# Kernel tuning notes

Hardware: AMD Instinct MI355X
Metric: run time of the kernel (lower is better)

The kernel has to match this reference:

```python
import jax, jax.numpy as jnp
import numpy as np
import math

B, T, D, H = 2, 2048, 1024, 16
HD = D // H
SOFTMAX_EPS = 1e-9
LN_EPS = 1e-5
NEG_INF = -1e9

def setup_inputs() -> dict:
    key = jax.random.key(0)
    ks = jax.random.split(key, 8)
    x = jax.random.normal(ks[0], (B, T, D), dtype=jnp.float32)
    # additive causal mask: 0 on/below diagonal, -1e9 above
    causal = jnp.where(jnp.tril(jnp.ones((T, T), dtype=bool)), 0.0, NEG_INF).astype(jnp.float32)
    attn_mask = jnp.broadcast_to(causal, (B, T, T))
    s = 0.02
    W_proj = jax.random.normal(ks[1], (D, 3 * D), dtype=jnp.float32) * s
    b_proj = jnp.zeros((3 * D,), dtype=jnp.float32)
    W_out = jax.random.normal(ks[2], (D, D), dtype=jnp.float32) * s
    b_out = jnp.zeros((D,), dtype=jnp.float32)
    ln_gamma = jnp.ones((D,), dtype=jnp.float32)
    ln_beta = jnp.zeros((D,), dtype=jnp.float32)
    return {"x": x, "attn_mask": attn_mask, "W_proj": W_proj, "b_proj": b_proj,
            "W_out": W_out, "b_out": b_out, "ln_gamma": ln_gamma, "ln_beta": ln_beta}

def reference(x, attn_mask, W_proj, b_proj, W_out, b_out, ln_gamma, ln_beta):
    Bv, Tv = x.shape[0], x.shape[1]
    qkv = x @ W_proj + b_proj                      # [B,T,3D]
    q, k, v = jnp.split(qkv, 3, axis=-1)
    q = q.reshape(Bv, Tv, H, HD).transpose(0, 2, 1, 3)  # [B,H,T,hd]
    k = k.reshape(Bv, Tv, H, HD).transpose(0, 2, 1, 3)
    v = v.reshape(Bv, Tv, H, HD).transpose(0, 2, 1, 3)
    # NOTE: mask added BEFORE scaling, matching the original module
    scores = (jnp.einsum('bhqd,bhkd->bhqk', q, k) + attn_mask[:, None, :, :]) / math.sqrt(HD)
    num = jnp.exp(scores)
    wts = num / (num.sum(axis=-1, keepdims=True) + SOFTMAX_EPS)  # eps-safe softmax, no max-subtract
    attn = jnp.einsum('bhqk,bhkd->bhqd', wts, v)   # [B,H,T,hd]
    y = attn.transpose(0, 2, 1, 3).reshape(Bv, Tv, D)
    z = x + y @ W_out + b_out
    mu = z.mean(axis=-1, keepdims=True)
    var = ((z - mu) ** 2).mean(axis=-1, keepdims=True)
    return (z - mu) / jnp.sqrt(var + LN_EPS) * ln_gamma + ln_beta
```

## Files before the change

kernel.cpp:

```cpp
#include <hip/hip_runtime.h>
#include <stdint.h>

typedef unsigned short u16;
typedef __attribute__((ext_vector_type(8))) short short8;
typedef __attribute__((ext_vector_type(4))) short sh4;
typedef __attribute__((ext_vector_type(4))) float f32x4;

#define MFMA16(a,b,c) __builtin_amdgcn_mfma_f32_16x16x32_bf16((a),(b),(c),0,0,0)

__device__ __forceinline__ u16 f2bf(float f) {
  union { float f; uint32_t u; } c; c.f = f;
  uint32_t u = c.u;
  return (u16)((u + 0x7fffu + ((u >> 16) & 1u)) >> 16);
}

__device__ __forceinline__ void async_cp16(const void* g, void* l) {
  __builtin_amdgcn_global_load_lds((__attribute__((address_space(1))) void*)g,
                                   (__attribute__((address_space(3))) void*)l,
                                   16, 0, 0);
}

__global__ __launch_bounds__(256) void prep(const float* __restrict__ x,
                                            const float* __restrict__ Wp,
                                            const float* __restrict__ Wo,
                                            u16* __restrict__ x_bf,
                                            u16* __restrict__ WpT,
                                            u16* __restrict__ WoT) {
  int bx = blockIdx.x;
  int t = threadIdx.x;
  if (bx < 4096) {
    int i = bx * 256 + t;
    float4 v = ((const float4*)x)[i];
    ushort4 o; o.x = f2bf(v.x); o.y = f2bf(v.y); o.z = f2bf(v.z); o.w = f2bf(v.w);
    ((ushort4*)x_bf)[i] = o;
    return;
  }
  __shared__ float tile[64][65];
  const float* in; u16* out; int C, blk;
  blk = bx - 4096;
  if (blk < 768) { in = Wp; out = WpT; C = 3072; }
  else           { in = Wo; out = WoT; C = 1024; blk -= 768; }
  const int R = 1024;
  int nbc = C >> 6;
  int c0 = (blk % nbc) << 6;
  int r0 = (blk / nbc) << 6;
  int li = t & 15;
  int hi = t >> 4;
  for (int i = 0; i < 4; i++) {
    int r = hi + (i << 4);
    float4 v = *(const float4*)&in[(size_t)(r0 + r) * C + c0 + (li << 2)];
    tile[r][(li << 2) + 0] = v.x;
    tile[r][(li << 2) + 1] = v.y;
    tile[r][(li << 2) + 2] = v.z;
    tile[r][(li << 2) + 3] = v.w;
  }
  __syncthreads();
  int rr4 = li << 2;
  for (int i = 0; i < 4; i++) {
    int col = hi + (i << 4);
    ushort4 o;
    o.x = f2bf(tile[rr4 + 0][col]);
    o.y = f2bf(tile[rr4 + 1][col]);
    o.z = f2bf(tile[rr4 + 2][col]);
    o.w = f2bf(tile[rr4 + 3][col]);
    *(ushort4*)&out[(size_t)(c0 + col) * R + r0 + rr4] = o;
  }
}

__global__ __launch_bounds__(256, 2) void gemm_qkv(
    const u16* __restrict__ A, const u16* __restrict__ Bt,
    const float* __restrict__ bias, u16* __restrict__ qkb, u16* __restrict__ Vtb) {
  __shared__ __align__(16) u16 As[8192];
  __shared__ __align__(16) u16 Bs[8192];
  int t = threadIdx.x;
  int w = t >> 6, lane = t & 63, quad = lane >> 4, l15 = lane & 15;
  int wr = w >> 1, wc = w & 1;
  int m0 = blockIdx.y * 128;
  int n0 = blockIdx.x * 128;
  bool isqk = (n0 < 2048);

  const u16* gA[4]; const u16* gB[4]; u16* lA[4]; u16* lB[4];
  {
    int rbase = t >> 2, cg = t & 3;
    for (int i = 0; i < 4; i++) {
      int r = rbase + (i & 1) * 64;
      int half = i >> 1;
      gA[i] = A + (size_t)(m0 + r) * 1024 + half * 32 + cg * 8;
      gB[i] = Bt + (size_t)(n0 + r) * 1024 + half * 32 + cg * 8;
      lA[i] = &As[half * 4096 + r * 32 + cg * 8];
      lB[i] = &Bs[half * 4096 + r * 32 + cg * 8];
    }
  }

  f32x4 acc[4][4];
  f32x4 zero = {0.f, 0.f, 0.f, 0.f};
  for (int mt = 0; mt < 4; mt++)
    for (int nt = 0; nt < 4; nt++) acc[mt][nt] = zero;

  for (int k0 = 0; k0 < 1024; k0 += 64) {
    __syncthreads();
    for (int i = 0; i < 4; i++) {
      async_cp16(gA[i] + k0, lA[i]);
      async_cp16(gB[i] + k0, lB[i]);
    }
    __syncthreads();
    for (int kc = 0; kc < 2; kc++) {
      short8 af[4], bf[4];
      int off = kc * 4096 + quad * 8;
      for (int mt = 0; mt < 4; mt++)
        af[mt] = *(const short8*)&As[off + (wr * 64 + mt * 16 + l15) * 32];
      for (int nt = 0; nt < 4; nt++)
        bf[nt] = *(const short8*)&Bs[off + (wc * 64 + nt * 16 + l15) * 32];
      if (isqk) {
        for (int mt = 0; mt < 4; mt++)
          for (int nt = 0; nt < 4; nt++)
            acc[mt][nt] = MFMA16(bf[nt], af[mt], acc[mt][nt]);
      } else {
        for (int mt = 0; mt < 4; mt++)
          for (int nt = 0; nt < 4; nt++)
            acc[mt][nt] = MFMA16(af[mt], bf[nt], acc[mt][nt]);
      }
    }
  }
  if (isqk) {
    for (int mt = 0; mt < 4; mt++) {
      int m = m0 + wr * 64 + mt * 16 + l15;
      for (int nt = 0; nt < 4; nt++) {
        int nb = n0 + wc * 64 + nt * 16 + quad * 4;
        float4 bv = *(const float4*)&bias[nb];
        ushort4 o;
        o.x = f2bf(acc[mt][nt][0] + bv.x);
        o.y = f2bf(acc[mt][nt][1] + bv.y);
        o.z = f2bf(acc[mt][nt][2] + bv.z);
        o.w = f2bf(acc[mt][nt][3] + bv.w);
        *(ushort4*)&qkb[(size_t)m * 2048 + nb] = o;
      }
    }
  } else {
    for (int nt = 0; nt < 4; nt++) {
      int n = n0 + wc * 64 + nt * 16 + l15;
      float bv = bias[n];
      int d = n - 2048;
      for (int mt = 0; mt < 4; mt++) {
        int mb = m0 + wr * 64 + mt * 16 + quad * 4;
        ushort4 o;
        o.x = f2bf(acc[mt][nt][0] + bv);
        o.y = f2bf(acc[mt][nt][1] + bv);
        o.z = f2bf(acc[mt][nt][2] + bv);
        o.w = f2bf(acc[mt][nt][3] + bv);
        *(ushort4*)&Vtb[(size_t)d * 4096 + mb] = o;
      }
    }
  }
}

__global__ __launch_bounds__(256, 2) void gemm_out_res(
    const u16* __restrict__ A, const u16* __restrict__ Bt,
    const float* __restrict__ bias, const float* __restrict__ X,
    float* __restrict__ Z) {
  __shared__ __align__(16) u16 As[8192];
  __shared__ __align__(16) u16 Bs[4096];
  int t = threadIdx.x;
  int w = t >> 6, lane = t & 63, quad = lane >> 4, l15 = lane & 15;
  int wr = w >> 1, wc = w & 1;
  int m0 = blockIdx.y * 128;
  int n0 = blockIdx.x * 64;

  const u16* gA[4]; u16* lA[4];
  const u16* gB[2]; u16* lB[2];
  {
    int rbase = t >> 2, cg = t & 3;
    for (int i = 0; i < 4; i++) {
      int r = rbase + (i & 1) * 64;
      int half = i >> 1;
      gA[i] = A + (size_t)(m0 + r) * 1024 + half * 32 + cg * 8;
      lA[i] = &As[half * 4096 + r * 32 + cg * 8];
    }
    for (int i = 0; i < 2; i++) {
      gB[i] = Bt + (size_t)(n0 + rbase) * 1024 + i * 32 + cg * 8;
      lB[i] = &Bs[i * 2048 + rbase * 32 + cg * 8];
    }
  }

  f32x4 acc[4][2];
  f32x4 zero = {0.f, 0.f, 0.f, 0.f};
  for (int mt = 0; mt < 4; mt++)
    for (int nt = 0; nt < 2; nt++) acc[mt][nt] = zero;

  for (int k0 = 0; k0 < 1024; k0 += 64) {
    __syncthreads();
    for (int i = 0; i < 4; i++) async_cp16(gA[i] + k0, lA[i]);
    for (int i = 0; i < 2; i++) async_cp16(gB[i] + k0, lB[i]);
    __syncthreads();
    for (int kc = 0; kc < 2; kc++) {
      short8 af[4], bf[2];
      for (int mt = 0; mt < 4; mt++)
        af[mt] = *(const short8*)&As[kc * 4096 + (wr * 64 + mt * 16 + l15) * 32 + quad * 8];
      for (int nt = 0; nt < 2; nt++)
        bf[nt] = *(const short8*)&Bs[kc * 2048 + (wc * 32 + nt * 16 + l15) * 32 + quad * 8];
      for (int mt = 0; mt < 4; mt++)
        for (int nt = 0; nt < 2; nt++)
          acc[mt][nt] = MFMA16(bf[nt], af[mt], acc[mt][nt]);
    }
  }
  for (int mt = 0; mt < 4; mt++) {
    int m = m0 + wr * 64 + mt * 16 + l15;
    for (int nt = 0; nt < 2; nt++) {
      int nb = n0 + wc * 32 + nt * 16 + quad * 4;
      float4 bv = *(const float4*)&bias[nb];
      size_t idx = (size_t)m * 1024 + nb;
      float4 xv = *(const float4*)&X[idx];
      float4 o;
      o.x = acc[mt][nt][0] + bv.x + xv.x;
      o.y = acc[mt][nt][1] + bv.y + xv.y;
      o.z = acc[mt][nt][2] + bv.z + xv.z;
      o.w = acc[mt][nt][3] + bv.w + xv.w;
      *(float4*)&Z[idx] = o;
    }
  }
}

#define LDP 68
__global__ __launch_bounds__(256, 2) void attn_v3(
    const u16* __restrict__ qk, const u16* __restrict__ Vt,
    u16* __restrict__ y) {
  __shared__ __align__(16) u16 K_lds[2][4096];
  __shared__ __align__(16) u16 V_lds[2][4096];
  __shared__ __align__(16) u16 P_lds[4 * 16 * LDP];
  int bx = blockIdx.x;
  int sub = bx >> 3;
  int bh = (bx & 7) * 4 + (sub >> 4);
  int slot = sub & 15;
  int h = bh & 15, b = bh >> 4;
  int t = threadIdx.x, w = t >> 6, lane = t & 63, quad = lane >> 4, l15 = lane & 15;
  size_t rowbase = (size_t)b * 2048;
  u16* Pw = P_lds + w * 16 * LDP;
  f32x4 zero = {0.f, 0.f, 0.f, 0.f};

  const u16 *Kg[2], *Vg[2];
  u16 *Kl[2][2], *Vl[2][2];
  for (int i = 0; i < 2; i++) {
    int c = t + 256 * i;
    int half = c >> 8, row = (c >> 2) & 63, cg = c & 3;
    int col = half * 32 + cg * 8;
    Kg[i] = qk + (rowbase + row) * 2048 + 1024 + h * 64 + col;
    Vg[i] = Vt + (size_t)(h * 64 + row) * 4096 + rowbase + col;
    Kl[0][i] = &K_lds[0][c * 8]; Kl[1][i] = &K_lds[1][c * 8];
    Vl[0][i] = &V_lds[0][c * 8]; Vl[1][i] = &V_lds[1][c * 8];
  }

  for (int i = 0; i < 2; i++) { async_cp16(Kg[i], Kl[0][i]); async_cp16(Vg[i], Vl[0][i]); }

  int cur = 0;
  for (int pass = 0; pass < 2; pass++) {
    int qt = pass ? (31 - slot) : slot;
    int q0 = qt * 64;
    short8 qf0, qf1;
    {
      const u16* qp = qk + (rowbase + q0 + w * 16 + l15) * 2048 + h * 64 + quad * 8;
      qf0 = *(const short8*)qp;
      qf1 = *(const short8*)(qp + 32);
    }
    f32x4 o[4];
    for (int nt = 0; nt < 4; nt++) o[nt] = zero;
    float rs[4] = {0.f, 0.f, 0.f, 0.f};

    for (int kt = 0; kt <= qt; kt++) {
      __syncthreads();
      int nxt = cur ^ 1;
      if (kt < qt) {
        size_t ko = (size_t)(kt + 1) * 64;
        for (int i = 0; i < 2; i++) {
          async_cp16(Kg[i] + ko * 2048, Kl[nxt][i]);
          async_cp16(Vg[i] + ko, Vl[nxt][i]);
        }
      } else if (pass == 0) {
        for (int i = 0; i < 2; i++) { async_cp16(Kg[i], Kl[nxt][i]); async_cp16(Vg[i], Vl[nxt][i]); }
      }
      const u16* Kb = K_lds[cur];
      const u16* Vb = V_lds[cur];
      f32x4 s[4];
      for (int nt = 0; nt < 4; nt++) {
        const u16* kr = Kb + (nt * 16 + l15) * 32 + quad * 8;
        f32x4 a2 = zero;
        a2 = MFMA16(qf0, *(const short8*)kr, a2);
        a2 = MFMA16(qf1, *(const short8*)(kr + 2048), a2);
        s[nt] = a2;
      }
      bool diag = (kt == qt);
      int qloc = w * 16 + quad * 4;
      for (int nt = 0; nt < 4; nt++) {
        int col = nt * 16 + l15;
        for (int r = 0; r < 4; r++) {
          float p = __expf(s[nt][r] * 0.125f);
          if (diag && col > qloc + r) p = 0.f;
          rs[r] += p;
          Pw[(quad * 4 + r) * LDP + col] = (u16)(__float_as_uint(p) >> 16);
        }
      }
      for (int c2 = 0; c2 < 2; c2++) {
        union { short8 v8; sh4 h2[2]; } u;
        u.h2[0] = *(const sh4*)&Pw[l15 * LDP + c2 * 32 + quad * 8];
        u.h2[1] = *(const sh4*)&Pw[l15 * LDP + c2 * 32 + quad * 8 + 4];
        for (int nt = 0; nt < 4; nt++) {
          const short8 bv = *(const short8*)&Vb[c2 * 2048 + (nt * 16 + l15) * 32 + quad * 8];
          o[nt] = MFMA16(u.v8, bv, o[nt]);
        }
      }
      cur = nxt;
    }
    for (int r = 0; r < 4; r++) {
      float v = rs[r];
      v += __shfl_xor(v, 1, 64);
      v += __shfl_xor(v, 2, 64);
      v += __shfl_xor(v, 4, 64);
      v += __shfl_xor(v, 8, 64);
      rs[r] = v;
    }
    for (int nt = 0; nt < 4; nt++) {
      for (int r = 0; r < 4; r++) {
        float ov = o[nt][r] / (rs[r] + 1e-9f);
        size_t qr = rowbase + q0 + w * 16 + quad * 4 + r;
        y[qr * 1024 + h * 64 + nt * 16 + l15] = f2bf(ov);
      }
    }
  }
}

__global__ __launch_bounds__(256) void ln_kernel(const float* __restrict__ Z,
                                                 const float* __restrict__ gamma,
                                                 const float* __restrict__ beta,
                                                 float* __restrict__ out) {
  int row = blockIdx.x;
  int t = threadIdx.x;
  float4 v = ((const float4*)(Z + (size_t)row * 1024))[t];
  float s = v.x + v.y + v.z + v.w;
  float s2 = v.x * v.x + v.y * v.y + v.z * v.z + v.w * v.w;
  for (int m = 1; m < 64; m <<= 1) {
    s += __shfl_xor(s, m, 64);
    s2 += __shfl_xor(s2, m, 64);
  }
  __shared__ float ss[4], ss2[4];
  int w = t >> 6;
  if ((t & 63) == 0) { ss[w] = s; ss2[w] = s2; }
  __syncthreads();
  s = ss[0] + ss[1] + ss[2] + ss[3];
  s2 = ss2[0] + ss2[1] + ss2[2] + ss2[3];
  float mu = s * (1.0f / 1024.0f);
  float var = s2 * (1.0f / 1024.0f) - mu * mu;
  float inv = rsqrtf(var + 1e-5f);
  float4 g = ((const float4*)gamma)[t];
  float4 bb = ((const float4*)beta)[t];
  float4 o;
  o.x = (v.x - mu) * inv * g.x + bb.x;
  o.y = (v.y - mu) * inv * g.y + bb.y;
  o.z = (v.z - mu) * inv * g.z + bb.z;
  o.w = (v.w - mu) * inv * g.w + bb.w;
  ((float4*)(out + (size_t)row * 1024))[t] = o;
}

extern "C" void kernel_launch(void* const* d_in, const int* in_sizes, int n_in,
                              void* d_out, int out_size, void* d_ws, size_t ws_size,
                              hipStream_t stream) {
  const float* x     = (const float*)d_in[0];
  const float* Wp    = (const float*)d_in[2];
  const float* bp    = (const float*)d_in[3];
  const float* Wo    = (const float*)d_in[4];
  const float* bo    = (const float*)d_in[5];
  const float* gamma = (const float*)d_in[6];
  const float* beta  = (const float*)d_in[7];
  float* out = (float*)d_out;

  char* ws = (char*)d_ws;
  u16*   x_bf = (u16*)(ws);
  u16*   WpT  = (u16*)(ws + 8388608);
  u16*   WoT  = (u16*)(ws + 14680064);
  u16*   qkb  = (u16*)(ws + 16777216);
  u16*   Vtb  = (u16*)(ws + 33554432);
  u16*   y    = (u16*)(ws + 41943040);
  float* z    = (float*)(ws + 50331648);

  prep<<<5120, 256, 0, stream>>>(x, Wp, Wo, x_bf, WpT, WoT);

  dim3 gqkv(24, 32);
  gemm_qkv<<<gqkv, 256, 0, stream>>>(x_bf, WpT, bp, qkb, Vtb);

  attn_v3<<<512, 256, 0, stream>>>(qkb, Vtb, y);

  dim3 go(16, 32);
  gemm_out_res<<<go, 256, 0, stream>>>(y, WoT, bo, x, z);

  ln_kernel<<<4096, 256, 0, stream>>>(z, gamma, beta, out);
}
```

Baseline: 222.1 us.

## Fold softmax scale into Q, use exp2, transpose score MFMA for packed P stores

```diff
diff --git a/kernel.cpp b/kernel.cpp
--- a/kernel.cpp
+++ b/kernel.cpp
@@ -12,6 +12,14 @@
   union { float f; uint32_t u; } c; c.f = f;
   uint32_t u = c.u;
   return (u16)((u + 0x7fffu + ((u >> 16) & 1u)) >> 16);
+}
+
+__device__ __forceinline__ float fast_exp2(float x) {
+#if __has_builtin(__builtin_amdgcn_exp2f)
+  return __builtin_amdgcn_exp2f(x);
+#else
+  return __expf(x * 0.69314718056f);
+#endif
 }
 
 __device__ __forceinline__ void async_cp16(const void* g, void* l) {
@@ -123,16 +131,17 @@
     }
   }
   if (isqk) {
+    float qscale = (n0 < 1024) ? 0.18033688011112042f : 1.0f;
     for (int mt = 0; mt < 4; mt++) {
       int m = m0 + wr * 64 + mt * 16 + l15;
       for (int nt = 0; nt < 4; nt++) {
         int nb = n0 + wc * 64 + nt * 16 + quad * 4;
         float4 bv = *(const float4*)&bias[nb];
         ushort4 o;
-        o.x = f2bf(acc[mt][nt][0] + bv.x);
-        o.y = f2bf(acc[mt][nt][1] + bv.y);
-        o.z = f2bf(acc[mt][nt][2] + bv.z);
-        o.w = f2bf(acc[mt][nt][3] + bv.w);
+        o.x = f2bf((acc[mt][nt][0] + bv.x) * qscale);
+        o.y = f2bf((acc[mt][nt][1] + bv.y) * qscale);
+        o.z = f2bf((acc[mt][nt][2] + bv.z) * qscale);
+        o.w = f2bf((acc[mt][nt][3] + bv.w) * qscale);
         *(ushort4*)&qkb[(size_t)m * 2048 + nb] = o;
       }
     }
@@ -220,13 +229,14 @@
   }
 }
 
-#define LDP 68
-__global__ __launch_bounds__(256, 2) void attn_v3(
+#define LDPK 72
+__global__ __launch_bounds__(256, 2) void attn_v5(
     const u16* __restrict__ qk, const u16* __restrict__ Vt,
     u16* __restrict__ y) {
   __shared__ __align__(16) u16 K_lds[2][4096];
   __shared__ __align__(16) u16 V_lds[2][4096];
-  __shared__ __align__(16) u16 P_lds[4 * 16 * LDP];
+  __shared__ __align__(16) u16 P_lds[4 * 16 * LDPK];
+  __shared__ float rs_sh[4][16];
   int bx = blockIdx.x;
   int sub = bx >> 3;
   int bh = (bx & 7) * 4 + (sub >> 4);
@@ -234,7 +244,7 @@
   int h = bh & 15, b = bh >> 4;
   int t = threadIdx.x, w = t >> 6, lane = t & 63, quad = lane >> 4, l15 = lane & 15;
   size_t rowbase = (size_t)b * 2048;
-  u16* Pw = P_lds + w * 16 * LDP;
+  u16* Pw = P_lds + w * 16 * LDPK;
   f32x4 zero = {0.f, 0.f, 0.f, 0.f};
 
   const u16 *Kg[2], *Vg[2];
@@ -263,7 +273,7 @@
     }
     f32x4 o[4];
     for (int nt = 0; nt < 4; nt++) o[nt] = zero;
-    float rs[4] = {0.f, 0.f, 0.f, 0.f};
+    float rsl = 0.f;
 
     for (int kt = 0; kt <= qt; kt++) {
       __syncthreads();
@@ -283,43 +293,47 @@
       for (int nt = 0; nt < 4; nt++) {
         const u16* kr = Kb + (nt * 16 + l15) * 32 + quad * 8;
         f32x4 a2 = zero;
-        a2 = MFMA16(qf0, *(const short8*)kr, a2);
-        a2 = MFMA16(qf1, *(const short8*)(kr + 2048), a2);
+        a2 = MFMA16(*(const short8*)kr, qf0, a2);
+        a2 = MFMA16(*(const short8*)(kr + 2048), qf1, a2);
         s[nt] = a2;
       }
       bool diag = (kt == qt);
-      int qloc = w * 16 + quad * 4;
+      int qg = w * 16 + l15;
       for (int nt = 0; nt < 4; nt++) {
-        int col = nt * 16 + l15;
-        for (int r = 0; r < 4; r++) {
-          float p = __expf(s[nt][r] * 0.125f);
-          if (diag && col > qloc + r) p = 0.f;
-          rs[r] += p;
-          Pw[(quad * 4 + r) * LDP + col] = (u16)(__float_as_uint(p) >> 16);
+        int kl = nt * 16 + quad * 4;
+        float p0 = fast_exp2(s[nt][0]);
+        float p1 = fast_exp2(s[nt][1]);
+        float p2 = fast_exp2(s[nt][2]);
+        float p3 = fast_exp2(s[nt][3]);
+        if (diag) {
+          if (kl + 0 > qg) p0 = 0.f;
+          if (kl + 1 > qg) p1 = 0.f;
+          if (kl + 2 > qg) p2 = 0.f;
+          if (kl + 3 > qg) p3 = 0.f;
         }
+        rsl += (p0 + p1) + (p2 + p3);
+        uint32_t w0 = __builtin_amdgcn_perm(__float_as_uint(p1), __float_as_uint(p0), 0x07060302u);
+        uint32_t w1 = __builtin_amdgcn_perm(__float_as_uint(p3), __float_as_uint(p2), 0x07060302u);
+        uint2 pk; pk.x = w0; pk.y = w1;
+        *(uint2*)&Pw[l15 * LDPK + kl] = pk;
       }
       for (int c2 = 0; c2 < 2; c2++) {
-        union { short8 v8; sh4 h2[2]; } u;
-        u.h2[0] = *(const sh4*)&Pw[l15 * LDP + c2 * 32 + quad * 8];
-        u.h2[1] = *(const sh4*)&Pw[l15 * LDP + c2 * 32 + quad * 8 + 4];
+        short8 af = *(const short8*)&Pw[l15 * LDPK + c2 * 32 + quad * 8];
         for (int nt = 0; nt < 4; nt++) {
           const short8 bv = *(const short8*)&Vb[c2 * 2048 + (nt * 16 + l15) * 32 + quad * 8];
-          o[nt] = MFMA16(u.v8, bv, o[nt]);
+          o[nt] = MFMA16(af, bv, o[nt]);
         }
       }
       cur = nxt;
     }
-    for (int r = 0; r < 4; r++) {
-      float v = rs[r];
-      v += __shfl_xor(v, 1, 64);
-      v += __shfl_xor(v, 2, 64);
-      v += __shfl_xor(v, 4, 64);
-      v += __shfl_xor(v, 8, 64);
-      rs[r] = v;
-    }
+    rsl += __shfl_xor(rsl, 16, 64);
+    rsl += __shfl_xor(rsl, 32, 64);
+    if (lane < 16) rs_sh[w][lane] = rsl;
+    float rq[4];
+    for (int r = 0; r < 4; r++) rq[r] = rs_sh[w][quad * 4 + r] + 1e-9f;
     for (int nt = 0; nt < 4; nt++) {
       for (int r = 0; r < 4; r++) {
-        float ov = o[nt][r] / (rs[r] + 1e-9f);
+        float ov = o[nt][r] / rq[r];
         size_t qr = rowbase + q0 + w * 16 + quad * 4 + r;
         y[qr * 1024 + h * 64 + nt * 16 + l15] = f2bf(ov);
       }
@@ -385,7 +399,7 @@
   dim3 gqkv(24, 32);
   gemm_qkv<<<gqkv, 256, 0, stream>>>(x_bf, WpT, bp, qkb, Vtb);
 
-  attn_v3<<<512, 256, 0, stream>>>(qkb, Vtb, y);
+  attn_v5<<<512, 256, 0, stream>>>(qkb, Vtb, y);
 
   dim3 go(16, 32);
   gemm_out_res<<<go, 256, 0, stream>>>(y, WoT, bo, x, z);
```

Measured after the change: 215.1 us. 1.03x faster.
